# Kernel optimization log

Measured on AMD Instinct MI355X. Metric: run time of the kernel, lower is better.

## Reference

```python
import jax, jax.numpy as jnp
import numpy as np

N, C, WP, H, W = 2, 64, 64, 240, 320
NB, K = 6, 3  # num_bases, input_ks
EPS = 1e-5


def _conv(x, w, pad):
    return jax.lax.conv_general_dilated(
        x, w, (1, 1), [(pad, pad), (pad, pad)],
        dimension_numbers=('NCHW', 'OIHW', 'NCHW'))


def _bn(x, g, b, m, v):
    # eval-mode BatchNorm2d with running stats
    inv = g * jax.lax.rsqrt(v + EPS)
    return x * inv[None, :, None, None] + (b - m * inv)[None, :, None, None]


def _forward(feat, weight, w1, b1, w2, b2, coef, coef_bias,
             br_gamma, br_beta, br_mean, br_var,
             w3, bn3_gamma, bn3_beta, bn3_mean, bn3_var):
    n, c, h, w = feat.shape
    # conv_bases: Basic2d (3x3 conv + bias + relu) then 1x1 conv -> K*K*NB channels
    cat = jnp.concatenate([feat, weight], axis=1)
    t = jax.nn.relu(_conv(cat, w1, 1) + b1[None, :, None, None])
    bases = _conv(t, w2, 0) + b2[None, :, None, None]          # [N, NB*K*K, H, W]
    bases = bases.reshape(n, NB, K * K, h, w)                   # [N, NB, L, H, W]
    # F.unfold: im2col patches, channel-major (C outer, kh*kw inner) like torch
    patches = jax.lax.conv_general_dilated_patches(
        feat, (K, K), (1, 1), [(1, 1), (1, 1)],
        dimension_numbers=('NCHW', 'OIHW', 'NCHW'))             # [N, C*K*K, H, W]
    patches = patches.reshape(n, c, K * K, h, w)                # [N, C, L, H, W]
    # dynamic per-pixel basis combination
    bases_out = jnp.einsum('bmlhw,bclhw->bcmhw', bases, patches)
    bases_out = bases_out.reshape(n, c * NB, h, w)              # [N, C*NB, H, W]
    # 1x1 conv with coef + bias
    out = _conv(bases_out, coef, 0) + coef_bias[None, :, None, None]
    # br: BN + ReLU
    out = jax.nn.relu(_bn(out, br_gamma, br_beta, br_mean, br_var))
    # conv3: Basic2d with BN (3x3 conv no bias + BN + ReLU)
    out = _conv(out, w3, 1)
    out = jax.nn.relu(_bn(out, bn3_gamma, bn3_beta, bn3_mean, bn3_var))
    return out


def setup_inputs() -> dict:
    key = jax.random.key(0)
    ks = jax.random.split(key, 8)
    f = lambda i, s, sc: jax.random.normal(ks[i], s, dtype=jnp.float32) * sc
    return {
        'feat': f(0, (N, C, H, W), 1.0),
        'weight': f(1, (N, WP, H, W), 1.0),
        'w1': f(2, (C, C + WP, 3, 3), 0.05),
        'b1': jnp.zeros((C,), jnp.float32),
        'w2': f(3, (K * K * NB, C, 1, 1), 0.05),
        'b2': jnp.zeros((K * K * NB,), jnp.float32),
        'coef': f(4, (C, C * NB, 1, 1), 0.05),
        'coef_bias': jnp.zeros((C,), jnp.float32),
        'br_gamma': jnp.ones((C,), jnp.float32),
        'br_beta': jnp.zeros((C,), jnp.float32),
        'br_mean': jnp.zeros((C,), jnp.float32),
        'br_var': jnp.ones((C,), jnp.float32),
        'w3': f(5, (C, C, 3, 3), 0.05),
        'bn3_gamma': jnp.ones((C,), jnp.float32),
        'bn3_beta': jnp.zeros((C,), jnp.float32),
        'bn3_mean': jnp.zeros((C,), jnp.float32),
        'bn3_var': jnp.ones((C,), jnp.float32),
    }


def reference(feat, weight, w1, b1, w2, b2, coef, coef_bias,
              br_gamma, br_beta, br_mean, br_var,
              w3, bn3_gamma, bn3_beta, bn3_mean, bn3_var):
    return _forward(feat, weight, w1, b1, w2, b2, coef, coef_bias,
                    br_gamma, br_beta, br_mean, br_var,
                    w3, bn3_gamma, bn3_beta, bn3_mean, bn3_var)
```

## Files before the change

### kernel.cpp

```cpp
#include <hip/hip_runtime.h>
#include <math.h>

#define HH 240
#define WW 320
#define HWSZ (240*320)
#define NN 2

#define OFF_BW1   0
#define OFF_BW3   147456
#define OFF_W2A   221184
#define OFF_COEFA 229376
#define OFF_BN    278528
#define OFF_FHF   279552
#define OFF_FHW   19940352

typedef __attribute__((ext_vector_type(8))) _Float16 half8v;
typedef __attribute__((ext_vector_type(4))) _Float16 half4v;
typedef __attribute__((ext_vector_type(4))) float f32x4;
typedef __attribute__((ext_vector_type(2))) float f32x2;

__device__ __forceinline__ half8v h8zero() {
    half8v z;
    #pragma unroll
    for (int j = 0; j < 8; ++j) z[j] = (_Float16)0.f;
    return z;
}

__global__ void prep_k(const float* __restrict__ w1, const float* __restrict__ w3,
                       const float* __restrict__ w2, const float* __restrict__ coef,
                       const float* __restrict__ coef_bias,
                       const float* __restrict__ brg, const float* __restrict__ brb,
                       const float* __restrict__ brm, const float* __restrict__ brv,
                       const float* __restrict__ g3, const float* __restrict__ b3,
                       const float* __restrict__ m3, const float* __restrict__ v3,
                       float* __restrict__ ws) {
    int id = blockIdx.x * 256 + threadIdx.x;
    _Float16* hw = (_Float16*)ws;

    if (id < 9216) {
        int l = id & 63; int f = id >> 6;
        int m = f & 3;   int g = f >> 2;
        int t = g % 9, cc = g / 9;
        _Float16* dst = hw + OFF_BW1/2 + (size_t)(g*4 + m)*512 + l*8;
        #pragma unroll
        for (int j = 0; j < 8; ++j) {
            int ci = cc*32 + (l>>4)*8 + j;
            int co = m*16 + (l&15);
            dst[j] = (_Float16)w1[(co*128 + ci)*9 + t];
        }
        return;
    }
    id -= 9216;
    if (id < 4608) {
        int l = id & 63; int f = id >> 6;
        int m = f & 3;   int g = f >> 2;
        int t = g % 9, cc = g / 9;
        _Float16* dst = hw + OFF_BW3/2 + (size_t)(g*4 + m)*512 + l*8;
        #pragma unroll
        for (int j = 0; j < 8; ++j) {
            int ci = cc*32 + (l>>4)*8 + j;
            int co = m*16 + (l&15);
            dst[j] = (_Float16)w3[(co*64 + ci)*9 + t];
        }
        return;
    }
    id -= 4608;
    if (id < 512) {
        int l = id & 63; int f = id >> 6;
        int mf = f & 3, kc = f >> 2;
        int row = mf*16 + (l & 15);
        _Float16* dst = hw + OFF_W2A/2 + (size_t)((kc*4 + mf)*64 + l)*8;
        #pragma unroll
        for (int j = 0; j < 8; ++j) {
            int k = kc*32 + (l>>4)*8 + j;
            dst[j] = (row < 54) ? (_Float16)w2[row*64 + k] : (_Float16)0.f;
        }
        return;
    }
    id -= 512;
    if (id < 3072) {
        int l = id & 63; int f = id >> 6;
        int ocf = f & 3; int g2 = f >> 2;
        int ch = g2 % 3, cg = g2 / 3;
        int oc = ocf*16 + (l & 15);
        _Float16* dst = hw + OFF_COEFA/2 + (size_t)((g2*4 + ocf)*64 + l)*8;
        #pragma unroll
        for (int j = 0; j < 8; ++j) {
            int k32 = (l>>4)*8 + j;
            int m = ch*2 + (k32 >> 4);
            int c = cg*16 + (k32 & 15);
            dst[j] = (_Float16)coef[oc*384 + c*6 + m];
        }
        return;
    }
    id -= 3072;
    if (id < 64) {
        float s = brg[id] * rsqrtf(brv[id] + 1e-5f);
        ws[OFF_BN/4 + id]      = s;
        ws[OFF_BN/4 + 64 + id] = coef_bias[id]*s + brb[id] - brm[id]*s;
        return;
    }
    id -= 64;
    if (id < 64) {
        float s = g3[id] * rsqrtf(v3[id] + 1e-5f);
        ws[OFF_BN/4 + 128 + id] = s;
        ws[OFF_BN/4 + 192 + id] = b3[id] - m3[id]*s;
    }
}

__global__ void nhwc_k(const float* __restrict__ feat, const float* __restrict__ wgt,
                       _Float16* __restrict__ fhf, _Float16* __restrict__ fhw) {
    __shared__ float L[64][65];
    const int tid = threadIdx.x;
    const int xb = blockIdx.x * 64, y = blockIdx.y;
    const int n = blockIdx.z >> 1, w = blockIdx.z & 1;
    const float* src = (w ? wgt : feat) + (size_t)n*64*HWSZ + y*WW + xb;
    _Float16* dst = (w ? fhw : fhf) + ((size_t)n*HWSZ + y*WW + xb) * 64;
    const int lx = tid & 63, c4 = tid >> 6;
    #pragma unroll
    for (int k = 0; k < 16; ++k) {
        int c = c4*16 + k;
        L[c][lx] = src[(size_t)c*HWSZ + lx];
    }
    __syncthreads();
    const int x = tid >> 3, c0 = (tid & 7) * 8;
    #pragma unroll
    for (int h = 0; h < 2; ++h) {
        int xx = x + h*32;
        half8v v;
        #pragma unroll
        for (int j = 0; j < 8; ++j) v[j] = (_Float16)L[c0 + j][xx];
        *(half8v*)&dst[xx*64 + c0] = v;
    }
}

template<int CHUNKS, bool HAS_SCALE>
__launch_bounds__(256, 2)
__global__ void convmfma_k(const _Float16* __restrict__ in0, const _Float16* __restrict__ in1,
                           const _Float16* __restrict__ wfr,
                           const float* __restrict__ epiA, const float* __restrict__ epiB,
                           float* __restrict__ outF, _Float16* __restrict__ outH) {
    __shared__ alignas(16) _Float16 TILE[180*40];
    __shared__ alignas(16) _Float16 WLDS[36*512];
    const int tid = threadIdx.x;
    const int lane = tid & 63, wv = tid >> 6;
    const int l15 = lane & 15, l4 = lane >> 4;
    const int x0 = blockIdx.x * 16, y0 = blockIdx.y * 8;
    const int nb = blockIdx.z;

    f32x4 acc[4][2];
    #pragma unroll
    for (int m = 0; m < 4; ++m)
        #pragma unroll
        for (int nf = 0; nf < 2; ++nf)
            acc[m][nf] = (f32x4){0.f, 0.f, 0.f, 0.f};

    #pragma unroll 1
    for (int cc = 0; cc < CHUNKS; ++cc) {
        __syncthreads();
        const _Float16* wsrc = wfr + (size_t)cc * 18432;
        #pragma unroll
        for (int j = 0; j < 9; ++j) {
            int seg = wv*9 + j;
            __builtin_amdgcn_global_load_lds(
                (const __attribute__((address_space(1))) unsigned int*)(wsrc + seg*512 + lane*8),
                (__attribute__((address_space(3))) unsigned int*)&WLDS[seg*512],
                16, 0, 0);
        }
        const _Float16* tens = (cc < 2) ? in0 : in1;
        const int choff = (cc & 1) * 32;
        const _Float16* base = tens + (size_t)nb * HWSZ * 64;
        #pragma unroll
        for (int it = 0; it < 3; ++it) {
            int task = tid + it*256;
            if (it < 2 || task < 720) {
                int pos = task >> 2, hh = task & 3;
                int py = pos / 18, px = pos - py*18;
                int gy = y0 - 1 + py, gx = x0 - 1 + px;
                bool ok = (gy >= 0) & (gy < HH) & (gx >= 0) & (gx < WW);
                half8v v = h8zero();
                if (ok) v = *(const half8v*)&base[((size_t)(gy*WW + gx))*64 + choff + hh*8];
                *(half8v*)&TILE[pos*40 + hh*8] = v;
            }
        }
        __syncthreads();

        #pragma unroll
        for (int t = 0; t < 9; ++t) {
            half8v Wm[4];
            #pragma unroll
            for (int m = 0; m < 4; ++m)
                Wm[m] = *(const half8v*)&WLDS[(t*4 + m)*512 + lane*8];
            const int ky = t / 3, kx = t - ky*3;
            #pragma unroll
            for (int nf = 0; nf < 2; ++nf) {
                int pos = (wv*2 + nf + ky)*18 + l15 + kx;
                half8v Ph = *(const half8v*)&TILE[pos*40 + l4*8];
                #pragma unroll
                for (int m = 0; m < 4; ++m)
                    acc[m][nf] = __builtin_amdgcn_mfma_f32_16x16x32_f16(Wm[m], Ph, acc[m][nf], 0, 0, 0);
            }
        }
    }

    if (HAS_SCALE) {
        #pragma unroll
        for (int m = 0; m < 4; ++m)
            #pragma unroll
            for (int i = 0; i < 4; ++i) {
                int co = m*16 + l4*4 + i;
                float sc = epiA[co], ofs = epiB[co];
                float* op = outF + (size_t)(nb*64 + co) * HWSZ;
                #pragma unroll
                for (int nf = 0; nf < 2; ++nf) {
                    int y = y0 + wv*2 + nf, x = x0 + l15;
                    op[y*WW + x] = fmaxf(acc[m][nf][i]*sc + ofs, 0.f);
                }
            }
    } else {
        #pragma unroll
        for (int nf = 0; nf < 2; ++nf) {
            int y = y0 + wv*2 + nf, x = x0 + l15;
            _Float16* op = outH + ((size_t)nb*HWSZ + y*WW + x) * 64;
            #pragma unroll
            for (int m = 0; m < 4; ++m) {
                half4v hv;
                #pragma unroll
                for (int i = 0; i < 4; ++i) {
                    float v = acc[m][nf][i] + epiA[m*16 + l4*4 + i];
                    hv[i] = (_Float16)fmaxf(v, 0.f);
                }
                *(half4v*)&op[m*16 + l4*4] = hv;
            }
        }
    }
}

__launch_bounds__(256, 1)
__global__ void fuse2_k(const _Float16* __restrict__ fhf, const _Float16* __restrict__ tH,
                        const _Float16* __restrict__ w2a,
                        const float* __restrict__ b2,
                        const _Float16* __restrict__ coefa,
                        const float* __restrict__ bn,
                        _Float16* __restrict__ uH) {
    __shared__ _Float16 BSH[128*56];
    __shared__ float PT[2][180*18];
    const int tid = threadIdx.x;
    const int lane = tid & 63, wv = tid >> 6;
    const int l15 = lane & 15, l4 = lane >> 4;
    const int x0 = blockIdx.x*16, y0 = blockIdx.y*8;
    const int nb = blockIdx.z;

    int s_pos[2], s_gy[2], s_gx[2], s_oct[2];
    bool s_ok[2], s_act[2];
    #pragma unroll
    for (int it = 0; it < 2; ++it) {
        int task = tid + it*256;
        s_act[it] = (task < 360);
        int pos = task >> 1, oct = task & 1;
        int py = pos / 18, pxx = pos - py*18;
        int gy = y0 - 1 + py, gx = x0 - 1 + pxx;
        s_pos[it] = pos; s_oct[it] = oct;
        s_gy[it] = gy; s_gx[it] = gx;
        s_ok[it] = (gy >= 0) & (gy < HH) & (gx >= 0) & (gx < WW) & s_act[it];
    }
    const _Float16* fbase = fhf + (size_t)nb * HWSZ * 64;

    half8v sv0 = h8zero(), sv1 = h8zero();
    if (s_ok[0]) sv0 = *(const half8v*)&fbase[((size_t)(s_gy[0]*WW + s_gx[0]))*64 + s_oct[0]*8];
    if (s_ok[1]) sv1 = *(const half8v*)&fbase[((size_t)(s_gy[1]*WW + s_gx[1]))*64 + s_oct[1]*8];

    half8v w2f[2][4];
    #pragma unroll
    for (int kc = 0; kc < 2; ++kc)
        #pragma unroll
        for (int mf = 0; mf < 4; ++mf)
            w2f[kc][mf] = *(const half8v*)(w2a + (size_t)((kc*4 + mf)*64 + lane)*8);

    f32x4 b2v[4];
    #pragma unroll
    for (int mf = 0; mf < 4; ++mf)
        #pragma unroll
        for (int i = 0; i < 4; ++i) {
            int row = mf*16 + l4*4 + i;
            b2v[mf][i] = (row < 54) ? b2[row] : 0.f;
        }

    #pragma unroll
    for (int nf = 0; nf < 2; ++nf) {
        int r = wv*2 + nf;
        int y = y0 + r, x = x0 + l15;
        const _Float16* tp = tH + ((size_t)nb*HWSZ + y*WW + x) * 64;
        half8v tf0 = *(const half8v*)&tp[l4*8];
        half8v tf1 = *(const half8v*)&tp[32 + l4*8];
        int px = r*16 + l15;
        #pragma unroll
        for (int mf = 0; mf < 4; ++mf) {
            f32x4 ab = (f32x4){0.f, 0.f, 0.f, 0.f};
            ab = __builtin_amdgcn_mfma_f32_16x16x32_f16(w2f[0][mf], tf0, ab, 0, 0, 0);
            ab = __builtin_amdgcn_mfma_f32_16x16x32_f16(w2f[1][mf], tf1, ab, 0, 0, 0);
            if (mf < 3 || l4 < 2) {
                half4v hv;
                #pragma unroll
                for (int i = 0; i < 4; ++i)
                    hv[i] = (_Float16)(ab[i] + b2v[mf][i]);
                *(half4v*)&BSH[px*56 + mf*16 + l4*4] = hv;
            }
        }
    }

    const int m0 = l4 >> 1;
    const int c08 = (l4 & 1) * 8;
    #pragma unroll
    for (int it = 0; it < 2; ++it) {
        half8v hv = it ? sv1 : sv0;
        if (s_act[it]) {
            float* dst = &PT[0][s_pos[it]*18 + s_oct[it]*8];
            #pragma unroll
            for (int q = 0; q < 4; ++q) {
                f32x2 v2;
                v2[0] = (float)hv[2*q];
                v2[1] = (float)hv[2*q + 1];
                *(f32x2*)(dst + 2*q) = v2;
            }
        }
    }
    __syncthreads();

    f32x4 acc[4][2];
    #pragma unroll
    for (int m = 0; m < 4; ++m)
        #pragma unroll
        for (int nf = 0; nf < 2; ++nf)
            acc[m][nf] = (f32x4){0.f, 0.f, 0.f, 0.f};

    #pragma unroll 1
    for (int cg = 0; cg < 4; ++cg) {
        half8v nv0 = h8zero(), nv1 = h8zero();
        if (cg < 3) {
            int chb = (cg + 1)*16;
            if (s_ok[0]) nv0 = *(const half8v*)&fbase[((size_t)(s_gy[0]*WW + s_gx[0]))*64 + chb + s_oct[0]*8];
            if (s_ok[1]) nv1 = *(const half8v*)&fbase[((size_t)(s_gy[1]*WW + s_gx[1]))*64 + chb + s_oct[1]*8];
        }

        half8v CA[3][4];
        #pragma unroll
        for (int ch = 0; ch < 3; ++ch)
            #pragma unroll
            for (int oc = 0; oc < 4; ++oc)
                CA[ch][oc] = *(const half8v*)(coefa + (size_t)(((cg*3 + ch)*4 + oc)*64 + lane)*8);

        const float* PTc = &PT[cg & 1][0];

        #pragma unroll
        for (int nf = 0; nf < 2; ++nf) {
            int r = wv*2 + nf;
            int px = r*16 + l15;
            float s[3][8];
            #pragma unroll
            for (int ch = 0; ch < 3; ++ch)
                #pragma unroll
                for (int j = 0; j < 8; ++j) s[ch][j] = 0.f;

            #pragma unroll
            for (int tap = 0; tap < 9; ++tap) {
                int ky = tap / 3, kx = tap - ky*3;
                int pos = (r + ky)*18 + l15 + kx;
                const float* pp = &PTc[pos*18 + c08];
                f32x2 p0 = *(const f32x2*)pp;
                f32x2 p1 = *(const f32x2*)(pp + 2);
                f32x2 p2 = *(const f32x2*)(pp + 4);
                f32x2 p3 = *(const f32x2*)(pp + 6);
                float ba0 = (float)BSH[px*56 + (m0*9 + tap)];
                float ba1 = (float)BSH[px*56 + ((m0 + 2)*9 + tap)];
                float ba2 = (float)BSH[px*56 + ((m0 + 4)*9 + tap)];
                float pv[8] = {p0[0], p0[1], p1[0], p1[1], p2[0], p2[1], p3[0], p3[1]};
                #pragma unroll
                for (int j = 0; j < 8; ++j) {
                    s[0][j] = fmaf(ba0, pv[j], s[0][j]);
                    s[1][j] = fmaf(ba1, pv[j], s[1][j]);
                    s[2][j] = fmaf(ba2, pv[j], s[2][j]);
                }
            }
            half8v B0, B1, B2;
            #pragma unroll
            for (int j = 0; j < 8; ++j) {
                B0[j] = (_Float16)s[0][j];
                B1[j] = (_Float16)s[1][j];
                B2[j] = (_Float16)s[2][j];
            }
            #pragma unroll
            for (int oc = 0; oc < 4; ++oc) {
                acc[oc][nf] = __builtin_amdgcn_mfma_f32_16x16x32_f16(CA[0][oc], B0, acc[oc][nf], 0, 0, 0);
                acc[oc][nf] = __builtin_amdgcn_mfma_f32_16x16x32_f16(CA[1][oc], B1, acc[oc][nf], 0, 0, 0);
                acc[oc][nf] = __builtin_amdgcn_mfma_f32_16x16x32_f16(CA[2][oc], B2, acc[oc][nf], 0, 0, 0);
            }
        }

        if (cg < 3) {
            #pragma unroll
            for (int it = 0; it < 2; ++it) {
                half8v hv = it ? nv1 : nv0;
                if (s_act[it]) {
                    float* dst = &PT[(cg + 1) & 1][s_pos[it]*18 + s_oct[it]*8];
                    #pragma unroll
                    for (int q = 0; q < 4; ++q) {
                        f32x2 v2;
                        v2[0] = (float)hv[2*q];
                        v2[1] = (float)hv[2*q + 1];
                        *(f32x2*)(dst + 2*q) = v2;
                    }
                }
            }
            __syncthreads();
        }
    }

    #pragma unroll
    for (int nf = 0; nf < 2; ++nf) {
        int y = y0 + wv*2 + nf, x = x0 + l15;
        _Float16* up = uH + ((size_t)nb*HWSZ + y*WW + x) * 64;
        #pragma unroll
        for (int ocf = 0; ocf < 4; ++ocf) {
            half4v hv;
            #pragma unroll
            for (int i = 0; i < 4; ++i) {
                int co = ocf*16 + l4*4 + i;
                hv[i] = (_Float16)fmaxf(acc[ocf][nf][i]*bn[co] + bn[64 + co], 0.f);
            }
            *(half4v*)&up[ocf*16 + l4*4] = hv;
        }
    }
}

extern "C" void kernel_launch(void* const* d_in, const int* in_sizes, int n_in,
                              void* d_out, int out_size, void* d_ws, size_t ws_size,
                              hipStream_t stream) {
    const float* feat      = (const float*)d_in[0];
    const float* wgt       = (const float*)d_in[1];
    const float* w1        = (const float*)d_in[2];
    const float* b1        = (const float*)d_in[3];
    const float* w2        = (const float*)d_in[4];
    const float* b2        = (const float*)d_in[5];
    const float* coef      = (const float*)d_in[6];
    const float* coef_bias = (const float*)d_in[7];
    const float* brg       = (const float*)d_in[8];
    const float* brb       = (const float*)d_in[9];
    const float* brm       = (const float*)d_in[10];
    const float* brv       = (const float*)d_in[11];
    const float* w3        = (const float*)d_in[12];
    const float* g3        = (const float*)d_in[13];
    const float* b3        = (const float*)d_in[14];
    const float* m3        = (const float*)d_in[15];
    const float* v3        = (const float*)d_in[16];

    float* out = (float*)d_out;
    _Float16* tH = (_Float16*)d_out;
    float* ws  = (float*)d_ws;
    _Float16* hw = (_Float16*)ws;
    _Float16* FHf = hw + OFF_FHF/2;
    _Float16* FHw = hw + OFF_FHW/2;

    prep_k<<<69, 256, 0, stream>>>(w1, w3, w2, coef, coef_bias,
                                   brg, brb, brm, brv, g3, b3, m3, v3, ws);

    nhwc_k<<<dim3(5, 240, 4), 256, 0, stream>>>(feat, wgt, FHf, FHw);

    dim3 grid(WW/16, HH/8, NN);

    convmfma_k<4, false><<<grid, 256, 0, stream>>>(
        FHf, FHw, hw + OFF_BW1/2, b1, b1, nullptr, tH);

    fuse2_k<<<grid, 256, 0, stream>>>(FHf, tH,
        hw + OFF_W2A/2, b2, hw + OFF_COEFA/2, ws + OFF_BN/4, FHw);

    convmfma_k<2, true><<<grid, 256, 0, stream>>>(
        FHw, FHw, hw + OFF_BW3/2,
        ws + OFF_BN/4 + 128, ws + OFF_BN/4 + 192, out, nullptr);
}
```

Baseline: 124.5 us.

## Use packed fp16 FMA for per-pixel basis combination with fp16 LDS tiles

The patch tile in shared memory is now stored as fp16 instead of fp32, and the bases tile is re-laid out tap-major so the three basis values a lane needs come from one 8-byte read. The inner 9-tap combination accumulates with packed half2 multiply-adds instead of scalar fp32 FMAs. This cuts LDS footprint, conversion instructions and ALU work in the hot loop. The cost is fp16 accumulation over 9 taps, which loses precision, and the bases tile is now written with scattered scalar LDS stores.

```diff
diff --git a/kernel.cpp b/kernel.cpp
--- a/kernel.cpp
+++ b/kernel.cpp
@@ -16,8 +16,8 @@
 
 typedef __attribute__((ext_vector_type(8))) _Float16 half8v;
 typedef __attribute__((ext_vector_type(4))) _Float16 half4v;
+typedef __attribute__((ext_vector_type(2))) _Float16 half2v;
 typedef __attribute__((ext_vector_type(4))) float f32x4;
-typedef __attribute__((ext_vector_type(2))) float f32x2;
 
 __device__ __forceinline__ half8v h8zero() {
     half8v z;
@@ -243,8 +243,8 @@
                         const _Float16* __restrict__ coefa,
                         const float* __restrict__ bn,
                         _Float16* __restrict__ uH) {
-    __shared__ _Float16 BSH[128*56];
-    __shared__ float PT[2][180*18];
+    __shared__ alignas(16) _Float16 BSH[128*72];
+    __shared__ alignas(16) _Float16 PT[2][180*24];
     const int tid = threadIdx.x;
     const int lane = tid & 63, wv = tid >> 6;
     const int l15 = lane & 15, l4 = lane >> 4;
@@ -300,11 +300,13 @@
             ab = __builtin_amdgcn_mfma_f32_16x16x32_f16(w2f[0][mf], tf0, ab, 0, 0, 0);
             ab = __builtin_amdgcn_mfma_f32_16x16x32_f16(w2f[1][mf], tf1, ab, 0, 0, 0);
             if (mf < 3 || l4 < 2) {
-                half4v hv;
-                #pragma unroll
-                for (int i = 0; i < 4; ++i)
-                    hv[i] = (_Float16)(ab[i] + b2v[mf][i]);
-                *(half4v*)&BSH[px*56 + mf*16 + l4*4] = hv;
+                #pragma unroll
+                for (int i = 0; i < 4; ++i) {
+                    int jb = mf*16 + l4*4 + i;
+                    int m = jb / 9;
+                    int tap = jb - m*9;
+                    BSH[px*72 + tap*8 + (m & 1)*4 + (m >> 1)] = (_Float16)(ab[i] + b2v[mf][i]);
+                }
             }
         }
     }
@@ -313,17 +315,8 @@
     const int c08 = (l4 & 1) * 8;
     #pragma unroll
     for (int it = 0; it < 2; ++it) {
-        half8v hv = it ? sv1 : sv0;
-        if (s_act[it]) {
-            float* dst = &PT[0][s_pos[it]*18 + s_oct[it]*8];
-            #pragma unroll
-            for (int q = 0; q < 4; ++q) {
-                f32x2 v2;
-                v2[0] = (float)hv[2*q];
-                v2[1] = (float)hv[2*q + 1];
-                *(f32x2*)(dst + 2*q) = v2;
-            }
-        }
+        if (s_act[it])
+            *(half8v*)&PT[0][s_pos[it]*24 + s_oct[it]*8] = (it ? sv1 : sv0);
     }
     __syncthreads();
 
@@ -350,44 +343,42 @@
             for (int oc = 0; oc < 4; ++oc)
                 CA[ch][oc] = *(const half8v*)(coefa + (size_t)(((cg*3 + ch)*4 + oc)*64 + lane)*8);
 
-        const float* PTc = &PT[cg & 1][0];
+        const _Float16* PTc = &PT[cg & 1][0];
 
         #pragma unroll
         for (int nf = 0; nf < 2; ++nf) {
             int r = wv*2 + nf;
             int px = r*16 + l15;
-            float s[3][8];
+            half2v s2[3][4];
             #pragma unroll
             for (int ch = 0; ch < 3; ++ch)
                 #pragma unroll
-                for (int j = 0; j < 8; ++j) s[ch][j] = 0.f;
+                for (int q = 0; q < 4; ++q)
+                    s2[ch][q] = (half2v){(_Float16)0.f, (_Float16)0.f};
 
             #pragma unroll
             for (int tap = 0; tap < 9; ++tap) {
                 int ky = tap / 3, kx = tap - ky*3;
                 int pos = (r + ky)*18 + l15 + kx;
-                const float* pp = &PTc[pos*18 + c08];
-                f32x2 p0 = *(const f32x2*)pp;
-                f32x2 p1 = *(const f32x2*)(pp + 2);
-                f32x2 p2 = *(const f32x2*)(pp + 4);
-                f32x2 p3 = *(const f32x2*)(pp + 6);
-                float ba0 = (float)BSH[px*56 + (m0*9 + tap)];
-                float ba1 = (float)BSH[px*56 + ((m0 + 2)*9 + tap)];
-                float ba2 = (float)BSH[px*56 + ((m0 + 4)*9 + tap)];
-                float pv[8] = {p0[0], p0[1], p1[0], p1[1], p2[0], p2[1], p3[0], p3[1]};
-                #pragma unroll
-                for (int j = 0; j < 8; ++j) {
-                    s[0][j] = fmaf(ba0, pv[j], s[0][j]);
-                    s[1][j] = fmaf(ba1, pv[j], s[1][j]);
-                    s[2][j] = fmaf(ba2, pv[j], s[2][j]);
+                half8v pt = *(const half8v*)&PTc[pos*24 + c08];
+                half4v bv = *(const half4v*)&BSH[px*72 + tap*8 + m0*4];
+                half2v b0 = (half2v){bv[0], bv[0]};
+                half2v b1 = (half2v){bv[1], bv[1]};
+                half2v bx = (half2v){bv[2], bv[2]};
+                #pragma unroll
+                for (int q = 0; q < 4; ++q) {
+                    half2v pq = (half2v){pt[2*q], pt[2*q + 1]};
+                    s2[0][q] = pq * b0 + s2[0][q];
+                    s2[1][q] = pq * b1 + s2[1][q];
+                    s2[2][q] = pq * bx + s2[2][q];
                 }
             }
             half8v B0, B1, B2;
             #pragma unroll
-            for (int j = 0; j < 8; ++j) {
-                B0[j] = (_Float16)s[0][j];
-                B1[j] = (_Float16)s[1][j];
-                B2[j] = (_Float16)s[2][j];
+            for (int q = 0; q < 4; ++q) {
+                B0[2*q] = s2[0][q][0]; B0[2*q+1] = s2[0][q][1];
+                B1[2*q] = s2[1][q][0]; B1[2*q+1] = s2[1][q][1];
+                B2[2*q] = s2[2][q][0]; B2[2*q+1] = s2[2][q][1];
             }
             #pragma unroll
             for (int oc = 0; oc < 4; ++oc) {
@@ -400,17 +391,8 @@
         if (cg < 3) {
             #pragma unroll
             for (int it = 0; it < 2; ++it) {
-                half8v hv = it ? nv1 : nv0;
-                if (s_act[it]) {
-                    float* dst = &PT[(cg + 1) & 1][s_pos[it]*18 + s_oct[it]*8];
-                    #pragma unroll
-                    for (int q = 0; q < 4; ++q) {
-                        f32x2 v2;
-                        v2[0] = (float)hv[2*q];
-                        v2[1] = (float)hv[2*q + 1];
-                        *(f32x2*)(dst + 2*q) = v2;
-                    }
-                }
+                if (s_act[it])
+                    *(half8v*)&PT[(cg + 1) & 1][s_pos[it]*24 + s_oct[it]*8] = (it ? nv1 : nv0);
             }
             __syncthreads();
         }
```

Measured after the change: 111.7 us. -10.3%, faster.
